# Optimization experiments

Measured on AMD Instinct MI355X. Metric: run time of the kernel, lower is better.

Reference implementation:

```python
import jax, jax.numpy as jnp
import numpy as np

# Domain bounds and training nu-range (from init_kwargs)
X_MIN, X_MAX = -1.0, 1.0
Y_MIN, Y_MAX = -1.0, 1.0
T_MIN, T_MAX = 0.0, 1.0
NU_MIN, NU_MAX = 0.01, 0.1

LAYERS = [4, 256, 256, 256, 256, 2]
N = 16384  # collocation points


def setup_inputs() -> dict:
    key = jax.random.key(0)
    ks = jax.random.split(key, 4 + 2 * (len(LAYERS) - 1))
    inp = {
        'x': jax.random.uniform(ks[0], (N, 1), minval=X_MIN, maxval=X_MAX, dtype=jnp.float32),
        'y': jax.random.uniform(ks[1], (N, 1), minval=Y_MIN, maxval=Y_MAX, dtype=jnp.float32),
        't': jax.random.uniform(ks[2], (N, 1), minval=T_MIN, maxval=T_MAX, dtype=jnp.float32),
        'nu': jax.random.uniform(ks[3], (N, 1), minval=NU_MIN, maxval=NU_MAX, dtype=jnp.float32),
    }
    # glorot_normal weights, zero biases (keras Dense defaults)
    for i in range(len(LAYERS) - 1):
        fan_in, fan_out = LAYERS[i], LAYERS[i + 1]
        std = (2.0 / (fan_in + fan_out)) ** 0.5
        inp[f'W{i}'] = std * jax.random.normal(ks[4 + 2 * i], (fan_in, fan_out), dtype=jnp.float32)
        inp[f'b{i}'] = jnp.zeros((fan_out,), dtype=jnp.float32)
    return inp


def _net(pt, nu, params):
    """MLP forward for a single point. pt: (3,) = (x, y, t); nu: scalar. Returns (2,) = (u, v)."""
    x, y, t = pt[0], pt[1], pt[2]
    h = jnp.stack([
        2.0 * (x - X_MIN) / (X_MAX - X_MIN) - 1.0,
        2.0 * (y - Y_MIN) / (Y_MAX - Y_MIN) - 1.0,
        2.0 * (t - T_MIN) / (T_MAX - T_MIN) - 1.0,
        2.0 * (nu - NU_MIN) / (NU_MAX - NU_MIN) - 1.0,
    ])
    for W, b in params[:-1]:
        z = h @ W + b
        h = z * jax.nn.sigmoid(z)  # swish
    W, b = params[-1]
    return h @ W + b


def _residual_point(pt, nu, params):
    """Burgers PDE residual (f_u, f_v) at one collocation point via nested forward-mode AD."""
    f = lambda p: _net(p, nu, params)
    uv = f(pt)                          # (2,)
    J = jax.jacfwd(f)(pt)               # (2,3): d(u,v)/d(x,y,t)
    H = jax.jacfwd(jax.jacfwd(f))(pt)   # (2,3,3)
    u, v = uv[0], uv[1]
    u_x, u_y, u_t = J[0, 0], J[0, 1], J[0, 2]
    v_x, v_y, v_t = J[1, 0], J[1, 1], J[1, 2]
    u_xx, u_yy = H[0, 0, 0], H[0, 1, 1]
    v_xx, v_yy = H[1, 0, 0], H[1, 1, 1]
    f_u = u_t + u * u_x + v * u_y - nu * (u_xx + u_yy)
    f_v = v_t + u * v_x + v * v_y - nu * (v_xx + v_yy)
    return jnp.stack([f_u, f_v])


def reference(x, y, t, nu, W0, b0, W1, b1, W2, b2, W3, b3, W4, b4):
    params = [(W0, b0), (W1, b1), (W2, b2), (W3, b3), (W4, b4)]
    pts = jnp.concatenate([x, y, t], axis=1)  # (N, 3)
    res = jax.vmap(lambda p, n: _residual_point(p, n, params))(pts, nu[:, 0])
    return res  # (N, 2) = [f_u, f_v]
```

## Files before the change

kernel.cpp:

```cpp
#include <hip/hip_runtime.h>

typedef _Float16 f16;
typedef _Float16 v8hf __attribute__((ext_vector_type(8)));
typedef _Float16 v4hf __attribute__((ext_vector_type(4)));
typedef _Float16 v2hf __attribute__((ext_vector_type(2)));
typedef float    v4f  __attribute__((ext_vector_type(4)));

#define NPTS 16384
#define PTS  8
#define NLAYER_ELEMS 65536

__device__ __forceinline__ int swz(int m, int j) {
    return m * 256 + ((((j >> 3) ^ (m & 7)) << 3) | (j & 7));
}

__device__ __forceinline__ uint32_t pk_lo(float x0, float x1) {
    return __builtin_amdgcn_perm(__float_as_uint(x1), __float_as_uint(x0), 0x05040100u);
}
__device__ __forceinline__ uint32_t pk_hi(float x0, float x1) {
    return __builtin_amdgcn_perm(__float_as_uint(x1), __float_as_uint(x0), 0x07060302u);
}
__device__ __forceinline__ float up0(uint32_t lo, uint32_t hi) {
    return __uint_as_float(__builtin_amdgcn_perm(hi, lo, 0x05040100u));
}
__device__ __forceinline__ float up1(uint32_t lo, uint32_t hi) {
    return __uint_as_float(__builtin_amdgcn_perm(hi, lo, 0x07060302u));
}

__global__ void pack_weights(const float* __restrict__ W1, const float* __restrict__ W2,
                             const float* __restrict__ W3, f16* __restrict__ bh,
                             f16* __restrict__ bl) {
    const int L = blockIdx.x >> 3, ks = blockIdx.x & 7, n = threadIdx.x;
    const float* W = (L == 0) ? W1 : (L == 1) ? W2 : W3;
    f16 h[32], l[32];
    #pragma unroll
    for (int kk = 0; kk < 32; ++kk) {
        float w = W[(ks * 32 + kk) * 256 + n];
        f16 hh = (f16)w;
        h[kk] = hh;
        l[kk] = (f16)(w - (float)hh);
    }
    size_t off = (size_t)L * NLAYER_ELEMS + (size_t)(ks * 256 + n) * 32;
    #pragma unroll
    for (int i = 0; i < 4; ++i) {
        *(v8hf*)(bh + off + 8 * i) = *(v8hf*)(h + 8 * i);
        *(v8hf*)(bl + off + 8 * i) = *(v8hf*)(l + 8 * i);
    }
}

__global__ __launch_bounds__(256, 3) void pinn_burgers_kernel(
    const float* __restrict__ gx, const float* __restrict__ gy,
    const float* __restrict__ gt, const float* __restrict__ gnu,
    const float* __restrict__ W0, const float* __restrict__ b0,
    const float* __restrict__ b1, const float* __restrict__ b2,
    const float* __restrict__ b3,
    const float* __restrict__ W4, const float* __restrict__ b4,
    const f16* __restrict__ bh, const f16* __restrict__ bl,
    float* __restrict__ out)
{
    __shared__ f16 Ah[48 * 256];
    __shared__ f16 Al[48 * 256];
    __shared__ float red[PTS][12];
    __shared__ float pin[4][PTS];

    const int tid  = threadIdx.x;
    const int lane = tid & 63;
    const int wv   = tid >> 6;
    const int ln   = lane & 15;
    const int quad = lane >> 4;
    const int lnx  = ln & 7;
    const int p0   = blockIdx.x * PTS;

    if (tid < 4 * PTS) {
        int c = tid >> 3, p = tid & 7;
        const float* src = (c == 0) ? gx : (c == 1) ? gy : (c == 2) ? gt : gnu;
        pin[c][p] = src[p0 + p];
    }
    __syncthreads();

    const int pa    = lane >> 3;
    const int jb    = lane & 7;
    const int jbase = wv * 64 + jb * 8;

    auto store_split = [&](const float (&A)[8], int c) {
        v8hf hh, ll;
        #pragma unroll
        for (int e = 0; e < 8; ++e) {
            f16 hv = (f16)A[e];
            hh[e] = hv;
            ll[e] = (f16)(A[e] - (float)hv);
        }
        int idx = swz(c * PTS + pa, jbase);
        *(v8hf*)&Ah[idx] = hh;
        *(v8hf*)&Al[idx] = ll;
    };
    auto store_raw = [&](const float (&A)[8], int c) {
        uint4 lo, hi;
        lo.x = pk_lo(A[0], A[1]); lo.y = pk_lo(A[2], A[3]);
        lo.z = pk_lo(A[4], A[5]); lo.w = pk_lo(A[6], A[7]);
        hi.x = pk_hi(A[0], A[1]); hi.y = pk_hi(A[2], A[3]);
        hi.z = pk_hi(A[4], A[5]); hi.w = pk_hi(A[6], A[7]);
        int idx = swz(c * PTS + pa, jbase);
        *(uint4*)&Ah[idx] = lo;
        *(uint4*)&Al[idx] = hi;
    };

    {
        v4f w0v[2], w1v[2], w2v[2], w3v[2], bbv[2];
        #pragma unroll
        for (int h = 0; h < 2; ++h) {
            w0v[h] = *(const v4f*)(W0 +   0 + jbase + 4 * h);
            w1v[h] = *(const v4f*)(W0 + 256 + jbase + 4 * h);
            w2v[h] = *(const v4f*)(W0 + 512 + jbase + 4 * h);
            w3v[h] = *(const v4f*)(W0 + 768 + jbase + 4 * h);
            bbv[h] = *(const v4f*)(b0 + jbase + 4 * h);
        }
        float hx = pin[0][pa];
        float hy = pin[1][pa];
        float ht = 2.f * pin[2][pa] - 1.f;
        float hn = 2.f * (pin[3][pa] - 0.01f) * (1.f / 0.09f) - 1.f;
        float A0[8], A1[8], A2[8], A3[8], A4[8], A5[8];
        #pragma unroll
        for (int e = 0; e < 8; ++e) {
            float w0 = w0v[e >> 2][e & 3];
            float w1 = w1v[e >> 2][e & 3];
            float w2 = w2v[e >> 2][e & 3];
            float w3 = w3v[e >> 2][e & 3];
            float z  = hx * w0 + hy * w1 + ht * w2 + hn * w3 + bbv[e >> 2][e & 3];
            float zx = w0, zy = w1, zt = 2.f * w2;
            float s  = 1.f / (1.f + __expf(-z));
            float g1 = s * (1.f + z * (1.f - s));
            float g2 = s * (1.f - s) * (2.f + z * (1.f - 2.f * s));
            A0[e] = z * s;
            A1[e] = g1 * zx; A2[e] = g1 * zy; A3[e] = g1 * zt;
            A4[e] = g2 * zx * zx; A5[e] = g2 * zy * zy;
        }
        store_split(A0, 0); store_split(A1, 1); store_split(A2, 2);
        store_split(A3, 3); store_split(A4, 4); store_split(A5, 5);
    }
    __syncthreads();

    const float* bias_ptr[3] = { b1, b2, b3 };
    for (int L = 0; L < 3; ++L) {
        const f16* __restrict__ bhL = bh + (size_t)L * NLAYER_ELEMS;
        const f16* __restrict__ blL = bl + (size_t)L * NLAYER_ELEMS;
        const float* __restrict__ bv = bias_ptr[L];

        v4f acc[4][3];
        #pragma unroll
        for (int t = 0; t < 4; ++t)
            #pragma unroll
            for (int mt = 0; mt < 3; ++mt)
                acc[t][mt] = (v4f){0.f, 0.f, 0.f, 0.f};

        #pragma unroll 2
        for (int ks = 0; ks < 8; ++ks) {
            const int cb = (((4 * ks + quad) ^ lnx) << 3);
            v8hf a_h[3], a_l[3];
            #pragma unroll
            for (int mt = 0; mt < 3; ++mt) {
                const int rb = (mt * 16 + ln) * 256 + cb;
                a_h[mt] = *(const v8hf*)&Ah[rb];
                a_l[mt] = *(const v8hf*)&Al[rb];
            }
            v8hf w_h[4], w_l[4];
            #pragma unroll
            for (int t = 0; t < 4; ++t) {
                int n = wv * 64 + t * 16 + ln;
                size_t o = (size_t)(ks * 256 + n) * 32 + quad * 8;
                w_h[t] = *(const v8hf*)(bhL + o);
                w_l[t] = *(const v8hf*)(blL + o);
            }
            #pragma unroll
            for (int t = 0; t < 4; ++t)
                #pragma unroll
                for (int mt = 0; mt < 3; ++mt) {
                    acc[t][mt] = __builtin_amdgcn_mfma_f32_16x16x32_f16(w_h[t], a_h[mt], acc[t][mt], 0, 0, 0);
                    acc[t][mt] = __builtin_amdgcn_mfma_f32_16x16x32_f16(w_h[t], a_l[mt], acc[t][mt], 0, 0, 0);
                    acc[t][mt] = __builtin_amdgcn_mfma_f32_16x16x32_f16(w_l[t], a_h[mt], acc[t][mt], 0, 0, 0);
                }
        }
        __syncthreads();

        #pragma unroll
        for (int t = 0; t < 4; ++t)
            #pragma unroll
            for (int mt = 0; mt < 3; ++mt) {
                v4f a = acc[t][mt];
                int nb = wv * 64 + t * 16 + quad * 4;
                int m  = mt * 16 + ln;
                if (mt == 0 && ln < PTS) {
                    const float4 bq = *(const float4*)(bv + nb);
                    a[0] += bq.x; a[1] += bq.y; a[2] += bq.z; a[3] += bq.w;
                }
                int idx = swz(m, nb);
                uint2 lo, hi;
                lo.x = pk_lo(a[0], a[1]); lo.y = pk_lo(a[2], a[3]);
                hi.x = pk_hi(a[0], a[1]); hi.y = pk_hi(a[2], a[3]);
                *(uint2*)&Ah[idx] = lo;
                *(uint2*)&Al[idx] = hi;
            }

        {
            float z0[8], z1[8], z2[8], z3[8], z4[8], z5[8];
            auto load_z = [&](float (&Z)[8], int c) {
                int idx = swz(c * PTS + pa, jbase);
                uint4 lo = *(const uint4*)&Ah[idx];
                uint4 hi = *(const uint4*)&Al[idx];
                Z[0] = up0(lo.x, hi.x); Z[1] = up1(lo.x, hi.x);
                Z[2] = up0(lo.y, hi.y); Z[3] = up1(lo.y, hi.y);
                Z[4] = up0(lo.z, hi.z); Z[5] = up1(lo.z, hi.z);
                Z[6] = up0(lo.w, hi.w); Z[7] = up1(lo.w, hi.w);
            };
            load_z(z0, 0); load_z(z1, 1); load_z(z2, 2);
            load_z(z3, 3); load_z(z4, 4); load_z(z5, 5);

            float A0[8], g1[8], g2[8];
            #pragma unroll
            for (int e = 0; e < 8; ++e) {
                float zz = z0[e];
                float s  = 1.f / (1.f + __expf(-zz));
                A0[e] = zz * s;
                g1[e] = s * (1.f + zz * (1.f - s));
                g2[e] = s * (1.f - s) * (2.f + zz * (1.f - 2.f * s));
            }
            float A1[8], A2[8], A3[8], A4[8], A5[8];
            #pragma unroll
            for (int e = 0; e < 8; ++e) {
                A1[e] = g1[e] * z1[e];
                A2[e] = g1[e] * z2[e];
                A3[e] = g1[e] * z3[e];
                A4[e] = g2[e] * z1[e] * z1[e] + g1[e] * z4[e];
                A5[e] = g2[e] * z2[e] * z2[e] + g1[e] * z5[e];
            }
            if (L < 2) {
                store_split(A0, 0); store_split(A1, 1); store_split(A2, 2);
                store_split(A3, 3); store_split(A4, 4); store_split(A5, 5);
            } else {
                store_raw(A0, 0); store_raw(A1, 1); store_raw(A2, 2);
                store_raw(A3, 3); store_raw(A4, 4); store_raw(A5, 5);
            }
        }
        __syncthreads();
    }

    #pragma unroll
    for (int d = 0; d < 24; ++d) {
        int D  = wv * 24 + d;
        int p  = D / 12;
        int rm = D % 12;
        int c  = rm >> 1;
        int o  = rm & 1;
        int m  = c * PTS + p;
        int k0 = lane * 4;
        int idx = swz(m, k0);
        uint2 lo = *(const uint2*)&Ah[idx];
        uint2 hi = *(const uint2*)&Al[idx];
        float h0 = up0(lo.x, hi.x), h1 = up1(lo.x, hi.x);
        float h2 = up0(lo.y, hi.y), h3 = up1(lo.y, hi.y);
        float partial = h0 * W4[(k0 + 0) * 2 + o] + h1 * W4[(k0 + 1) * 2 + o]
                      + h2 * W4[(k0 + 2) * 2 + o] + h3 * W4[(k0 + 3) * 2 + o];
        #pragma unroll
        for (int off = 32; off > 0; off >>= 1)
            partial += __shfl_down(partial, off);
        if (lane == 0)
            red[p][rm] = partial + ((c == 0) ? b4[o] : 0.f);
    }
    __syncthreads();

    if (tid < PTS) {
        int p = tid;
        float u   = red[p][0],  v   = red[p][1];
        float ux  = red[p][2],  vx  = red[p][3];
        float uy  = red[p][4],  vy  = red[p][5];
        float ut  = red[p][6],  vt  = red[p][7];
        float uxx = red[p][8],  vxx = red[p][9];
        float uyy = red[p][10], vyy = red[p][11];
        float nuv = pin[3][p];
        float fu = ut + u * ux + v * uy - nuv * (uxx + uyy);
        float fv = vt + u * vx + v * vy - nuv * (vxx + vyy);
        out[(p0 + p) * 2 + 0] = fu;
        out[(p0 + p) * 2 + 1] = fv;
    }
}

extern "C" void kernel_launch(void* const* d_in, const int* in_sizes, int n_in,
                              void* d_out, int out_size, void* d_ws, size_t ws_size,
                              hipStream_t stream) {
    const float* x  = (const float*)d_in[0];
    const float* y  = (const float*)d_in[1];
    const float* t  = (const float*)d_in[2];
    const float* nu = (const float*)d_in[3];
    const float* W0 = (const float*)d_in[4];
    const float* b0 = (const float*)d_in[5];
    const float* W1 = (const float*)d_in[6];
    const float* b1 = (const float*)d_in[7];
    const float* W2 = (const float*)d_in[8];
    const float* b2 = (const float*)d_in[9];
    const float* W3 = (const float*)d_in[10];
    const float* b3 = (const float*)d_in[11];
    const float* W4 = (const float*)d_in[12];
    const float* b4 = (const float*)d_in[13];
    float* o = (float*)d_out;

    f16* bh = (f16*)d_ws;
    f16* bl = bh + 3 * (size_t)NLAYER_ELEMS;

    hipLaunchKernelGGL(pack_weights, dim3(24), dim3(256), 0, stream, W1, W2, W3, bh, bl);
    hipLaunchKernelGGL(pinn_burgers_kernel, dim3(NPTS / PTS), dim3(256), 0, stream,
                       x, y, t, nu, W0, b0, b1, b2, b3, W4, b4, bh, bl, o);
}
```

Baseline: 219.2 us.

## Double points per block to 16 with 512 threads and prefetch weight fragments

Each block now handles 16 points (96 activation rows) with 8 waves. Each wave covers 32 output columns across 6 M-tiles instead of 64 columns across 3, so every global weight fragment load feeds twice as many MFMAs. Weight fragments for the next k-step are double-buffered in registers so global loads overlap the MFMA work. Shared memory becomes dynamic at about 98KB per block, which raises register pressure and may lower occupancy.

```diff
diff --git a/kernel.cpp b/kernel.cpp
--- a/kernel.cpp
+++ b/kernel.cpp
@@ -7,7 +7,8 @@
 typedef float    v4f  __attribute__((ext_vector_type(4)));
 
 #define NPTS 16384
-#define PTS  8
+#define PTS  16
+#define ROWS 96
 #define NLAYER_ELEMS 65536
 
 __device__ __forceinline__ int swz(int m, int j) {
@@ -48,7 +49,7 @@
     }
 }
 
-__global__ __launch_bounds__(256, 3) void pinn_burgers_kernel(
+__global__ __launch_bounds__(512, 2) void pinn_burgers_kernel(
     const float* __restrict__ gx, const float* __restrict__ gy,
     const float* __restrict__ gt, const float* __restrict__ gnu,
     const float* __restrict__ W0, const float* __restrict__ b0,
@@ -58,10 +59,11 @@
     const f16* __restrict__ bh, const f16* __restrict__ bl,
     float* __restrict__ out)
 {
-    __shared__ f16 Ah[48 * 256];
-    __shared__ f16 Al[48 * 256];
-    __shared__ float red[PTS][12];
-    __shared__ float pin[4][PTS];
+    extern __shared__ char smem[];
+    f16*   Ah  = (f16*)smem;
+    f16*   Al  = Ah + ROWS * 256;
+    float* red = (float*)(Al + ROWS * 256);
+    float* pin = red + PTS * 12;
 
     const int tid  = threadIdx.x;
     const int lane = tid & 63;
@@ -72,15 +74,15 @@
     const int p0   = blockIdx.x * PTS;
 
     if (tid < 4 * PTS) {
-        int c = tid >> 3, p = tid & 7;
+        int c = tid >> 4, p = tid & 15;
         const float* src = (c == 0) ? gx : (c == 1) ? gy : (c == 2) ? gt : gnu;
-        pin[c][p] = src[p0 + p];
+        pin[c * PTS + p] = src[p0 + p];
     }
     __syncthreads();
 
-    const int pa    = lane >> 3;
-    const int jb    = lane & 7;
-    const int jbase = wv * 64 + jb * 8;
+    const int pa    = lane >> 2;
+    const int jb    = lane & 3;
+    const int jbase = wv * 32 + jb * 8;
 
     auto store_split = [&](const float (&A)[8], int c) {
         v8hf hh, ll;
@@ -115,10 +117,10 @@
             w3v[h] = *(const v4f*)(W0 + 768 + jbase + 4 * h);
             bbv[h] = *(const v4f*)(b0 + jbase + 4 * h);
         }
-        float hx = pin[0][pa];
-        float hy = pin[1][pa];
-        float ht = 2.f * pin[2][pa] - 1.f;
-        float hn = 2.f * (pin[3][pa] - 0.01f) * (1.f / 0.09f) - 1.f;
+        float hx = pin[0 * PTS + pa];
+        float hy = pin[1 * PTS + pa];
+        float ht = 2.f * pin[2 * PTS + pa] - 1.f;
+        float hn = 2.f * (pin[3 * PTS + pa] - 0.01f) * (1.f / 0.09f) - 1.f;
         float A0[8], A1[8], A2[8], A3[8], A4[8], A5[8];
         #pragma unroll
         for (int e = 0; e < 8; ++e) {
@@ -146,50 +148,61 @@
         const f16* __restrict__ blL = bl + (size_t)L * NLAYER_ELEMS;
         const float* __restrict__ bv = bias_ptr[L];
 
-        v4f acc[4][3];
-        #pragma unroll
-        for (int t = 0; t < 4; ++t)
-            #pragma unroll
-            for (int mt = 0; mt < 3; ++mt)
+        v4f acc[2][6];
+        #pragma unroll
+        for (int t = 0; t < 2; ++t)
+            #pragma unroll
+            for (int mt = 0; mt < 6; ++mt)
                 acc[t][mt] = (v4f){0.f, 0.f, 0.f, 0.f};
 
-        #pragma unroll 2
+        v8hf w_h[2][2], w_l[2][2];
+        #pragma unroll
+        for (int t = 0; t < 2; ++t) {
+            int n = wv * 32 + t * 16 + ln;
+            size_t o = (size_t)n * 32 + quad * 8;
+            w_h[0][t] = *(const v8hf*)(bhL + o);
+            w_l[0][t] = *(const v8hf*)(blL + o);
+        }
+
+        #pragma unroll
         for (int ks = 0; ks < 8; ++ks) {
+            const int cur = ks & 1, nxt = cur ^ 1;
+            if (ks + 1 < 8) {
+                #pragma unroll
+                for (int t = 0; t < 2; ++t) {
+                    int n = wv * 32 + t * 16 + ln;
+                    size_t o = (size_t)((ks + 1) * 256 + n) * 32 + quad * 8;
+                    w_h[nxt][t] = *(const v8hf*)(bhL + o);
+                    w_l[nxt][t] = *(const v8hf*)(blL + o);
+                }
+            }
             const int cb = (((4 * ks + quad) ^ lnx) << 3);
-            v8hf a_h[3], a_l[3];
-            #pragma unroll
-            for (int mt = 0; mt < 3; ++mt) {
+            v8hf a_h[6], a_l[6];
+            #pragma unroll
+            for (int mt = 0; mt < 6; ++mt) {
                 const int rb = (mt * 16 + ln) * 256 + cb;
                 a_h[mt] = *(const v8hf*)&Ah[rb];
                 a_l[mt] = *(const v8hf*)&Al[rb];
             }
-            v8hf w_h[4], w_l[4];
-            #pragma unroll
-            for (int t = 0; t < 4; ++t) {
-                int n = wv * 64 + t * 16 + ln;
-                size_t o = (size_t)(ks * 256 + n) * 32 + quad * 8;
-                w_h[t] = *(const v8hf*)(bhL + o);
-                w_l[t] = *(const v8hf*)(blL + o);
-            }
-            #pragma unroll
-            for (int t = 0; t < 4; ++t)
+            #pragma unroll
+            for (int t = 0; t < 2; ++t)
                 #pragma unroll
-                for (int mt = 0; mt < 3; ++mt) {
-                    acc[t][mt] = __builtin_amdgcn_mfma_f32_16x16x32_f16(w_h[t], a_h[mt], acc[t][mt], 0, 0, 0);
-                    acc[t][mt] = __builtin_amdgcn_mfma_f32_16x16x32_f16(w_h[t], a_l[mt], acc[t][mt], 0, 0, 0);
-                    acc[t][mt] = __builtin_amdgcn_mfma_f32_16x16x32_f16(w_l[t], a_h[mt], acc[t][mt], 0, 0, 0);
+                for (int mt = 0; mt < 6; ++mt) {
+                    acc[t][mt] = __builtin_amdgcn_mfma_f32_16x16x32_f16(w_h[cur][t], a_h[mt], acc[t][mt], 0, 0, 0);
+                    acc[t][mt] = __builtin_amdgcn_mfma_f32_16x16x32_f16(w_h[cur][t], a_l[mt], acc[t][mt], 0, 0, 0);
+                    acc[t][mt] = __builtin_amdgcn_mfma_f32_16x16x32_f16(w_l[cur][t], a_h[mt], acc[t][mt], 0, 0, 0);
                 }
         }
         __syncthreads();
 
         #pragma unroll
-        for (int t = 0; t < 4; ++t)
-            #pragma unroll
-            for (int mt = 0; mt < 3; ++mt) {
+        for (int t = 0; t < 2; ++t)
+            #pragma unroll
+            for (int mt = 0; mt < 6; ++mt) {
                 v4f a = acc[t][mt];
-                int nb = wv * 64 + t * 16 + quad * 4;
+                int nb = wv * 32 + t * 16 + quad * 4;
                 int m  = mt * 16 + ln;
-                if (mt == 0 && ln < PTS) {
+                if (mt == 0) {
                     const float4 bq = *(const float4*)(bv + nb);
                     a[0] += bq.x; a[1] += bq.y; a[2] += bq.z; a[3] += bq.w;
                 }
@@ -246,9 +259,9 @@
 
     #pragma unroll
     for (int d = 0; d < 24; ++d) {
-        int D  = wv * 24 + d;
-        int p  = D / 12;
-        int rm = D % 12;
+        int k  = d / 12;
+        int rm = d % 12;
+        int p  = wv * 2 + k;
         int c  = rm >> 1;
         int o  = rm & 1;
         int m  = c * PTS + p;
@@ -264,25 +277,27 @@
         for (int off = 32; off > 0; off >>= 1)
             partial += __shfl_down(partial, off);
         if (lane == 0)
-            red[p][rm] = partial + ((c == 0) ? b4[o] : 0.f);
+            red[p * 12 + rm] = partial + ((c == 0) ? b4[o] : 0.f);
     }
     __syncthreads();
 
     if (tid < PTS) {
         int p = tid;
-        float u   = red[p][0],  v   = red[p][1];
-        float ux  = red[p][2],  vx  = red[p][3];
-        float uy  = red[p][4],  vy  = red[p][5];
-        float ut  = red[p][6],  vt  = red[p][7];
-        float uxx = red[p][8],  vxx = red[p][9];
-        float uyy = red[p][10], vyy = red[p][11];
-        float nuv = pin[3][p];
+        float u   = red[p * 12 + 0],  v   = red[p * 12 + 1];
+        float ux  = red[p * 12 + 2],  vx  = red[p * 12 + 3];
+        float uy  = red[p * 12 + 4],  vy  = red[p * 12 + 5];
+        float ut  = red[p * 12 + 6],  vt  = red[p * 12 + 7];
+        float uxx = red[p * 12 + 8],  vxx = red[p * 12 + 9];
+        float uyy = red[p * 12 + 10], vyy = red[p * 12 + 11];
+        float nuv = pin[3 * PTS + p];
         float fu = ut + u * ux + v * uy - nuv * (uxx + uyy);
         float fv = vt + u * vx + v * vy - nuv * (vxx + vyy);
         out[(p0 + p) * 2 + 0] = fu;
         out[(p0 + p) * 2 + 1] = fv;
     }
 }
+
+#define SMEM_BYTES (ROWS * 256 * 2 * 2 + PTS * 12 * 4 + 4 * PTS * 4)
 
 extern "C" void kernel_launch(void* const* d_in, const int* in_sizes, int n_in,
                               void* d_out, int out_size, void* d_ws, size_t ws_size,
@@ -306,7 +321,14 @@
     f16* bh = (f16*)d_ws;
     f16* bl = bh + 3 * (size_t)NLAYER_ELEMS;
 
+    static bool s_attr_set = false;
+    if (!s_attr_set) {
+        hipFuncSetAttribute((const void*)pinn_burgers_kernel,
+                            hipFuncAttributeMaxDynamicSharedMemorySize, SMEM_BYTES);
+        s_attr_set = true;
+    }
+
     hipLaunchKernelGGL(pack_weights, dim3(24), dim3(256), 0, stream, W1, W2, W3, bh, bl);
-    hipLaunchKernelGGL(pinn_burgers_kernel, dim3(NPTS / PTS), dim3(256), 0, stream,
+    hipLaunchKernelGGL(pinn_burgers_kernel, dim3(NPTS / PTS), dim3(512), SMEM_BYTES, stream,
                        x, y, t, nu, W0, b0, b1, b2, b3, W4, b4, bh, bl, o);
 }
```

New measurement: 225.6 us. +2.9%, slower.
